# Performance work log

Hardware: AMD Instinct MI355X
Metric: run time of the kernel (lower is better)

The kernel has to match this reference:

```python
import jax, jax.numpy as jnp
import numpy as np

HIDDEN = 128
HEADS = 8
HEAD_DIM = HIDDEN // HEADS
N_BLOCKS = 2048
N_EDGES = 4096


def setup_inputs() -> dict:
    key = jax.random.key(0)
    ks = jax.random.split(key, 14)
    s = 0.02
    return {
        "block_features": jax.random.normal(ks[0], (N_BLOCKS, HIDDEN), dtype=jnp.float32),
        "edge_indices": jax.random.randint(ks[1], (2, N_EDGES), 0, N_BLOCKS, dtype=jnp.int32),
        # edge_encoder: Linear(2H->H), ReLU, Linear(H->H)
        "W_e1": jax.random.normal(ks[2], (2 * HIDDEN, HIDDEN), dtype=jnp.float32) * s,
        "b_e1": jnp.zeros((HIDDEN,), dtype=jnp.float32),
        "W_e2": jax.random.normal(ks[3], (HIDDEN, HIDDEN), dtype=jnp.float32) * s,
        "b_e2": jnp.zeros((HIDDEN,), dtype=jnp.float32),
        "Wq": jax.random.normal(ks[4], (HIDDEN, HIDDEN), dtype=jnp.float32) * s,
        "bq": jnp.zeros((HIDDEN,), dtype=jnp.float32),
        "Wk": jax.random.normal(ks[5], (HIDDEN, HIDDEN), dtype=jnp.float32) * s,
        "bk": jnp.zeros((HIDDEN,), dtype=jnp.float32),
        "Wv": jax.random.normal(ks[6], (HIDDEN, HIDDEN), dtype=jnp.float32) * s,
        "bv": jnp.zeros((HIDDEN,), dtype=jnp.float32),
        "Wo": jax.random.normal(ks[7], (HIDDEN, HIDDEN), dtype=jnp.float32) * s,
        "bo": jnp.zeros((HIDDEN,), dtype=jnp.float32),
    }


def reference(block_features, edge_indices, W_e1, b_e1, W_e2, b_e2,
              Wq, bq, Wk, bk, Wv, bv, Wo, bo):
    n_blocks = block_features.shape[0]
    src_idx, dst_idx = edge_indices[0], edge_indices[1]

    # gather src/dst node features, concat -> edge MLP (dropout is identity in eval)
    ef = jnp.concatenate([block_features[src_idx], block_features[dst_idx]], axis=1)  # [E, 2H]
    ef = jnp.maximum(ef @ W_e1 + b_e1, 0.0) @ W_e2 + b_e2  # [E, H]

    E = ef.shape[0]
    scale = HEAD_DIM ** -0.5
    q = (ef @ Wq + bq).reshape(E, HEADS, HEAD_DIM)
    k = (ef @ Wk + bk).reshape(E, HEADS, HEAD_DIM)
    v = (ef @ Wv + bv).reshape(E, HEADS, HEAD_DIM)

    # dense attention over all edges
    scores = jnp.einsum("ehd,fhd->hef", q, k) * scale  # [H, E, E]
    attn = jax.nn.softmax(scores, axis=-1)
    attn_out = jnp.einsum("hef,fhd->ehd", attn, v).reshape(E, HIDDEN)
    updated_edges = attn_out @ Wo + bo  # [E, H]

    # scatter_sum back to destination nodes
    block_updates = jax.ops.segment_sum(updated_edges, dst_idx, num_segments=n_blocks)
    return block_features + block_updates
```

## Files before the change

### kernel.cpp

```cpp
#include <hip/hip_runtime.h>
#include <hip/hip_bf16.h>

#define NB 2048
#define NE 4096
#define HID 128
#define NHEAD 8
#define HD 16

#define FPSCALE 1048576.0f
#define INV_FPSCALE (1.0f/1048576.0f)
#define QSCALE 0.36067376022224085f

typedef short s16x8 __attribute__((ext_vector_type(8)));
typedef float f32x4  __attribute__((ext_vector_type(4)));
typedef float f32x16 __attribute__((ext_vector_type(16)));

static __device__ __forceinline__ ushort f2bf(float x) {
    uint u = __builtin_bit_cast(uint, x);
    uint r = (u + 0x7fffu + ((u >> 16) & 1u)) >> 16;
    return (ushort)r;
}
static __device__ __forceinline__ uint pack2bf(float a, float b) {
    return (uint)f2bf(a) | ((uint)f2bf(b) << 16);
}
static __device__ __forceinline__ uint packrd(float a, float b) {
    uint ua = __builtin_bit_cast(uint, a) + 0x8000u;
    uint ub = __builtin_bit_cast(uint, b) + 0x8000u;
    return __builtin_amdgcn_perm(ub, ua, 0x07060302u);
}

__global__ __launch_bounds__(256) void convert_kernel(
    const float* __restrict__ We1, const float* __restrict__ We2,
    const float* __restrict__ Wq,  const float* __restrict__ Wk,
    const float* __restrict__ Wv,  const float* __restrict__ Wo,
    ushort* __restrict__ wb, int4* __restrict__ acc_zero)
{
    int i = blockIdx.x * 256 + threadIdx.x;
    if (i < 65536) acc_zero[i] = make_int4(0, 0, 0, 0);
    if (i < 32768) {
        int n = i >> 8, k = i & 255;
        wb[i] = f2bf(We1[k * HID + n]);
        return;
    }
    int j = i - 32768;
    int m = j >> 14;
    int r = j & 16383;
    int n = r >> 7, k = r & 127;
    const float* W = (m == 0) ? We2 : (m == 1) ? Wq : (m == 2) ? Wk : (m == 3) ? Wv : Wo;
    wb[i] = f2bf(W[k * HID + n]);
}

__global__ __launch_bounds__(512) void mlp_qkv_kernel(
    const float* __restrict__ bf, const int* __restrict__ src, const int* __restrict__ dst,
    const ushort* __restrict__ wb,
    const float* __restrict__ be1, const float* __restrict__ be2,
    const float* __restrict__ bq,  const float* __restrict__ bk, const float* __restrict__ bv,
    ushort* __restrict__ qg, ushort* __restrict__ kg, ushort* __restrict__ vT)
{
    __shared__ ushort sX[16][264];
    __shared__ ushort sH[16][136];
    __shared__ ushort sE[16][136];

    const int tid = threadIdx.x;
    const int w   = tid >> 6;
    const int l   = tid & 63;
    const int lo16 = l & 15;
    const int hi4  = l >> 4;
    const int e0 = blockIdx.x * 16;

    const ushort* We1T = wb;
    const ushort* We2T = wb + 32768;
    const ushort* WqT  = wb + 49152;
    const ushort* WkT  = wb + 65536;
    const ushort* WvT  = wb + 81920;

    {
        const int r  = tid >> 5;
        const int sg = tid & 31;
        const int e  = e0 + r;
        const int node = (sg < 16) ? src[e] : dst[e];
        const float4* rowp = (const float4*)(bf + node * HID);
        const int fb = (sg & 15) * 2;
        float4 t0 = rowp[fb], t1 = rowp[fb + 1];
        *(uint2*)&sX[r][sg * 8]     = make_uint2(pack2bf(t0.x, t0.y), pack2bf(t0.z, t0.w));
        *(uint2*)&sX[r][sg * 8 + 4] = make_uint2(pack2bf(t1.x, t1.y), pack2bf(t1.z, t1.w));
    }
    __syncthreads();

    f32x4 acc;

    {
        float b = be1[w * 16 + lo16];
        acc = (f32x4){b, b, b, b};
        #pragma unroll
        for (int k0 = 0; k0 < 8; k0++) {
            s16x8 a = *(const s16x8*)&sX[lo16][k0 * 32 + hi4 * 8];
            s16x8 bb = *(const s16x8*)(We1T + (w * 16 + lo16) * 256 + k0 * 32 + hi4 * 8);
            acc = __builtin_amdgcn_mfma_f32_16x16x32_bf16(a, bb, acc, 0, 0, 0);
        }
        #pragma unroll
        for (int r = 0; r < 4; r++)
            sH[hi4 * 4 + r][w * 16 + lo16] = f2bf(fmaxf(acc[r], 0.0f));
    }
    __syncthreads();

    {
        float b = be2[w * 16 + lo16];
        acc = (f32x4){b, b, b, b};
        #pragma unroll
        for (int k0 = 0; k0 < 4; k0++) {
            s16x8 a = *(const s16x8*)&sH[lo16][k0 * 32 + hi4 * 8];
            s16x8 bb = *(const s16x8*)(We2T + (w * 16 + lo16) * 128 + k0 * 32 + hi4 * 8);
            acc = __builtin_amdgcn_mfma_f32_16x16x32_bf16(a, bb, acc, 0, 0, 0);
        }
        #pragma unroll
        for (int r = 0; r < 4; r++)
            sE[hi4 * 4 + r][w * 16 + lo16] = f2bf(acc[r]);
    }
    __syncthreads();

#define PROJ(WT, BIAS, STORE) do { \
    float b_ = BIAS[w * 16 + lo16]; \
    acc = (f32x4){b_, b_, b_, b_}; \
    _Pragma("unroll") \
    for (int k0 = 0; k0 < 4; k0++) { \
        s16x8 a = *(const s16x8*)&sE[lo16][k0 * 32 + hi4 * 8]; \
        s16x8 bb = *(const s16x8*)(WT + (w * 16 + lo16) * 128 + k0 * 32 + hi4 * 8); \
        acc = __builtin_amdgcn_mfma_f32_16x16x32_bf16(a, bb, acc, 0, 0, 0); \
    } \
    _Pragma("unroll") \
    for (int r = 0; r < 4; r++) { STORE; } \
} while (0)

    PROJ(WqT, bq, { int e = e0 + hi4 * 4 + r;
                    qg[(w * NE + e) * 16 + lo16] = f2bf(acc[r] * QSCALE); });
    PROJ(WkT, bk, { int e = e0 + hi4 * 4 + r;
                    kg[(w * NE + e) * 16 + lo16] = f2bf(acc[r]); });
    PROJ(WvT, bv, { int e = e0 + hi4 * 4 + r;
                    vT[(w * 16 + lo16) * NE + e] = f2bf(acc[r]); });
#undef PROJ
}

__global__ __launch_bounds__(256) void attn_kernel(
    const ushort* __restrict__ qg, const ushort* __restrict__ kg,
    const ushort* __restrict__ vT, ushort* __restrict__ Og)
{
    __shared__ ushort P[4][2][8][32][4];
    __shared__ float sO[4][32][17];
    __shared__ float sL[4][2][32];

    const int tid = threadIdx.x;
    const int w   = tid >> 6;
    const int l   = tid & 63;
    const int h   = blockIdx.y;
    const int q0  = blockIdx.x * 32;
    const int lo16 = l & 15, hi4 = l >> 4;
    const int lo32 = l & 31, hi2 = l >> 5;

    const s16x8 qf = *(const s16x8*)(qg + (h * NE + q0 + lo32) * 16 + hi2 * 8);

    const f32x16 z16 = {0,0,0,0, 0,0,0,0, 0,0,0,0, 0,0,0,0};
    f32x4 o0 = {0,0,0,0}, o1 = {0,0,0,0};
    float L = 0.0f;

    const int kbase = w * (NE / 4);

    #pragma unroll 2
    for (int kt = 0; kt < NE / 4 / 32; kt++) {
        const int key0 = kbase + kt * 32;
        const int b = kt & 1;
        s16x8 kf = *(const s16x8*)(kg + (h * NE + key0 + lo32) * 16 + hi2 * 8);
        s16x8 vf = *(const s16x8*)(vT + (h * 16 + lo16) * NE + key0 + hi4 * 8);

        f32x16 s = __builtin_amdgcn_mfma_f32_32x32x16_bf16(kf, qf, z16, 0, 0, 0);

        float p[16];
        #pragma unroll
        for (int i = 0; i < 16; i++) { p[i] = __builtin_amdgcn_exp2f(s[i]); L += p[i]; }

        #pragma unroll
        for (int g = 0; g < 4; g++) {
            uint2 w2 = make_uint2(packrd(p[4*g], p[4*g+1]), packrd(p[4*g+2], p[4*g+3]));
            *(uint2*)&P[w][b][2*g + hi2][lo32][0] = w2;
        }

        uint2 alo = *(const uint2*)&P[w][b][2*hi4][lo16][0];
        uint2 ahi = *(const uint2*)&P[w][b][2*hi4 + 1][lo16][0];
        uint2 blo = *(const uint2*)&P[w][b][2*hi4][16 + lo16][0];
        uint2 bhi = *(const uint2*)&P[w][b][2*hi4 + 1][16 + lo16][0];
        uint4 ua = make_uint4(alo.x, alo.y, ahi.x, ahi.y);
        uint4 ub = make_uint4(blo.x, blo.y, bhi.x, bhi.y);
        s16x8 pb0 = __builtin_bit_cast(s16x8, ua);
        s16x8 pb1 = __builtin_bit_cast(s16x8, ub);
        o0 = __builtin_amdgcn_mfma_f32_16x16x32_bf16(vf, pb0, o0, 0, 0, 0);
        o1 = __builtin_amdgcn_mfma_f32_16x16x32_bf16(vf, pb1, o1, 0, 0, 0);
    }

    sL[w][hi2][lo32] = L;
    #pragma unroll
    for (int r = 0; r < 4; r++) {
        sO[w][lo16][hi4 * 4 + r]      = o0[r];
        sO[w][16 + lo16][hi4 * 4 + r] = o1[r];
    }
    __syncthreads();

    {
        const int q = tid >> 3;
        const int d0 = (tid & 7) * 2;
        float s0 = 0.0f, s1 = 0.0f, Lq = 0.0f;
        #pragma unroll
        for (int ww = 0; ww < 4; ww++) {
            s0 += sO[ww][q][d0];
            s1 += sO[ww][q][d0 + 1];
            Lq += sL[ww][0][q] + sL[ww][1][q];
        }
        float inv = 1.0f / Lq;
        *(uint*)&Og[(q0 + q) * HID + h * 16 + d0] = pack2bf(s0 * inv, s1 * inv);
    }
}

__global__ __launch_bounds__(512) void wo_scatter_kernel(
    const ushort* __restrict__ Og, const ushort* __restrict__ wb,
    const float* __restrict__ bo, const int* __restrict__ dst,
    int* __restrict__ acc_int)
{
    const int tid = threadIdx.x;
    const int w   = tid >> 6;
    const int l   = tid & 63;
    const int lo16 = l & 15, hi4 = l >> 4;
    const int e0 = blockIdx.x * 16;
    const ushort* WoT = wb + 98304;

    float b_ = bo[w * 16 + lo16];
    f32x4 acc = (f32x4){b_, b_, b_, b_};
    #pragma unroll
    for (int k0 = 0; k0 < 4; k0++) {
        s16x8 a = *(const s16x8*)(Og + (e0 + lo16) * HID + k0 * 32 + hi4 * 8);
        s16x8 bb = *(const s16x8*)(WoT + (w * 16 + lo16) * 128 + k0 * 32 + hi4 * 8);
        acc = __builtin_amdgcn_mfma_f32_16x16x32_bf16(a, bb, acc, 0, 0, 0);
    }

    #pragma unroll
    for (int r = 0; r < 4; r++) {
        int n = dst[e0 + hi4 * 4 + r];
        atomicAdd(acc_int + n * HID + w * 16 + lo16,
                  __float2int_rn(acc[r] * FPSCALE));
    }
}

__global__ __launch_bounds__(256) void finalize_kernel(
    const float4* __restrict__ bf, const int4* __restrict__ acc_int,
    float4* __restrict__ out)
{
    int i = blockIdx.x * 256 + threadIdx.x;
    float4 b = bf[i];
    int4   a = acc_int[i];
    out[i] = make_float4(b.x + (float)a.x * INV_FPSCALE,
                         b.y + (float)a.y * INV_FPSCALE,
                         b.z + (float)a.z * INV_FPSCALE,
                         b.w + (float)a.w * INV_FPSCALE);
}

extern "C" void kernel_launch(void* const* d_in, const int* in_sizes, int n_in,
                              void* d_out, int out_size, void* d_ws, size_t ws_size,
                              hipStream_t stream)
{
    const float* bf  = (const float*)d_in[0];
    const int*   ei  = (const int*)d_in[1];
    const int*   src = ei;
    const int*   dst = ei + NE;
    const float* We1 = (const float*)d_in[2];
    const float* be1 = (const float*)d_in[3];
    const float* We2 = (const float*)d_in[4];
    const float* be2 = (const float*)d_in[5];
    const float* Wq  = (const float*)d_in[6];
    const float* bq  = (const float*)d_in[7];
    const float* Wk  = (const float*)d_in[8];
    const float* bk  = (const float*)d_in[9];
    const float* Wv  = (const float*)d_in[10];
    const float* bv  = (const float*)d_in[11];
    const float* Wo  = (const float*)d_in[12];
    const float* bo  = (const float*)d_in[13];

    char* ws = (char*)d_ws;
    ushort* wb  = (ushort*)(ws);
    ushort* qg  = (ushort*)(ws + 229376);
    ushort* kg  = (ushort*)(ws + 229376 + (1u<<20));
    ushort* vT  = (ushort*)(ws + 229376 + (2u<<20));
    ushort* Og  = (ushort*)(ws + 229376 + (3u<<20));
    int*   acc  = (int*)  (ws + 229376 + (4u<<20));

    convert_kernel<<<448, 256, 0, stream>>>(We1, We2, Wq, Wk, Wv, Wo, wb, (int4*)acc);
    mlp_qkv_kernel<<<NE / 16, 512, 0, stream>>>(bf, src, dst, wb, be1, be2, bq, bk, bv,
                                                qg, kg, vT);
    attn_kernel<<<dim3(NE / 32, NHEAD), 256, 0, stream>>>(qg, kg, vT, Og);
    wo_scatter_kernel<<<NE / 16, 512, 0, stream>>>(Og, wb, bo, dst, acc);
    finalize_kernel<<<(NB * HID) / 1024, 256, 0, stream>>>((const float4*)bf, (const int4*)acc,
                                                           (float4*)d_out);
}
```

Measured before the change: 55.27 us.

## Compute softmax denominator via padded ones row in V MFMA, shuffle P in registers

V is stored transposed with 32 rows per head, where row 16 is filled with bf16 ones and the rest zero, so a single 32x32x16 MFMA yields both the P·V output and the row sum L. The P tile is rearranged into the MFMA B-operand layout through cross-half wave shuffles instead of an LDS round trip. The attention block grows to 8 waves, each covering 512 keys. This removes the scalar L accumulation and the per-iteration LDS traffic, at the cost of MFMA work on padding rows and twice the V storage.

```diff
diff --git a/kernel.cpp b/kernel.cpp
--- a/kernel.cpp
+++ b/kernel.cpp
@@ -33,10 +33,15 @@
     const float* __restrict__ We1, const float* __restrict__ We2,
     const float* __restrict__ Wq,  const float* __restrict__ Wk,
     const float* __restrict__ Wv,  const float* __restrict__ Wo,
-    ushort* __restrict__ wb, int4* __restrict__ acc_zero)
+    ushort* __restrict__ wb, int4* __restrict__ acc_zero, uint4* __restrict__ vfill)
 {
     int i = blockIdx.x * 256 + threadIdx.x;
-    if (i < 65536) acc_zero[i] = make_int4(0, 0, 0, 0);
+    if (i < 65536) {
+        acc_zero[i] = make_int4(0, 0, 0, 0);
+        int h = i >> 13, rr = (i >> 9) & 15, c = i & 511;
+        uint v = (rr == 0) ? 0x3f803f80u : 0u;
+        vfill[(h * 32 + 16 + rr) * 512 + c] = make_uint4(v, v, v, v);
+    }
     if (i < 32768) {
         int n = i >> 8, k = i & 255;
         wb[i] = f2bf(We1[k * HID + n]);
@@ -55,7 +60,7 @@
     const ushort* __restrict__ wb,
     const float* __restrict__ be1, const float* __restrict__ be2,
     const float* __restrict__ bq,  const float* __restrict__ bk, const float* __restrict__ bv,
-    ushort* __restrict__ qg, ushort* __restrict__ kg, ushort* __restrict__ vT)
+    ushort* __restrict__ qg, ushort* __restrict__ kg, ushort* __restrict__ vTx)
 {
     __shared__ ushort sX[16][264];
     __shared__ ushort sH[16][136];
@@ -137,85 +142,98 @@
     PROJ(WkT, bk, { int e = e0 + hi4 * 4 + r;
                     kg[(w * NE + e) * 16 + lo16] = f2bf(acc[r]); });
     PROJ(WvT, bv, { int e = e0 + hi4 * 4 + r;
-                    vT[(w * 16 + lo16) * NE + e] = f2bf(acc[r]); });
+                    vTx[(w * 32 + lo16) * NE + e] = f2bf(acc[r]); });
 #undef PROJ
 }
 
-__global__ __launch_bounds__(256) void attn_kernel(
+__global__ __launch_bounds__(512) void attn_kernel(
     const ushort* __restrict__ qg, const ushort* __restrict__ kg,
-    const ushort* __restrict__ vT, ushort* __restrict__ Og)
-{
-    __shared__ ushort P[4][2][8][32][4];
-    __shared__ float sO[4][32][17];
-    __shared__ float sL[4][2][32];
+    const ushort* __restrict__ vTx, ushort* __restrict__ Og)
+{
+    __shared__ float sO[8][32][18];
 
     const int tid = threadIdx.x;
     const int w   = tid >> 6;
     const int l   = tid & 63;
+    const int lo32 = l & 31, hi2 = l >> 5;
     const int h   = blockIdx.y;
     const int q0  = blockIdx.x * 32;
-    const int lo16 = l & 15, hi4 = l >> 4;
-    const int lo32 = l & 31, hi2 = l >> 5;
 
     const s16x8 qf = *(const s16x8*)(qg + (h * NE + q0 + lo32) * 16 + hi2 * 8);
-
-    const f32x16 z16 = {0,0,0,0, 0,0,0,0, 0,0,0,0, 0,0,0,0};
-    f32x4 o0 = {0,0,0,0}, o1 = {0,0,0,0};
-    float L = 0.0f;
-
-    const int kbase = w * (NE / 4);
+    const ushort* vbase = vTx + (size_t)(h * 32 + lo32) * NE + hi2 * 8;
+
+    const f32x16 z16 = {};
+    f32x16 accO = {};
 
     #pragma unroll 2
-    for (int kt = 0; kt < NE / 4 / 32; kt++) {
-        const int key0 = kbase + kt * 32;
-        const int b = kt & 1;
-        s16x8 kf = *(const s16x8*)(kg + (h * NE + key0 + lo32) * 16 + hi2 * 8);
-        s16x8 vf = *(const s16x8*)(vT + (h * 16 + lo16) * NE + key0 + hi4 * 8);
+    for (int kt = 0; kt < 16; kt++) {
+        const int key0 = w * 512 + kt * 32;
+        s16x8 kf  = *(const s16x8*)(kg + (h * NE + key0 + lo32) * 16 + hi2 * 8);
+        s16x8 va0 = *(const s16x8*)(vbase + key0);
+        s16x8 va1 = *(const s16x8*)(vbase + key0 + 16);
 
         f32x16 s = __builtin_amdgcn_mfma_f32_32x32x16_bf16(kf, qf, z16, 0, 0, 0);
 
-        float p[16];
-        #pragma unroll
-        for (int i = 0; i < 16; i++) { p[i] = __builtin_amdgcn_exp2f(s[i]); L += p[i]; }
-
-        #pragma unroll
-        for (int g = 0; g < 4; g++) {
-            uint2 w2 = make_uint2(packrd(p[4*g], p[4*g+1]), packrd(p[4*g+2], p[4*g+3]));
-            *(uint2*)&P[w][b][2*g + hi2][lo32][0] = w2;
-        }
-
-        uint2 alo = *(const uint2*)&P[w][b][2*hi4][lo16][0];
-        uint2 ahi = *(const uint2*)&P[w][b][2*hi4 + 1][lo16][0];
-        uint2 blo = *(const uint2*)&P[w][b][2*hi4][16 + lo16][0];
-        uint2 bhi = *(const uint2*)&P[w][b][2*hi4 + 1][16 + lo16][0];
-        uint4 ua = make_uint4(alo.x, alo.y, ahi.x, ahi.y);
-        uint4 ub = make_uint4(blo.x, blo.y, bhi.x, bhi.y);
-        s16x8 pb0 = __builtin_bit_cast(s16x8, ua);
-        s16x8 pb1 = __builtin_bit_cast(s16x8, ub);
-        o0 = __builtin_amdgcn_mfma_f32_16x16x32_bf16(vf, pb0, o0, 0, 0, 0);
-        o1 = __builtin_amdgcn_mfma_f32_16x16x32_bf16(vf, pb1, o1, 0, 0, 0);
-    }
-
-    sL[w][hi2][lo32] = L;
-    #pragma unroll
-    for (int r = 0; r < 4; r++) {
-        sO[w][lo16][hi4 * 4 + r]      = o0[r];
-        sO[w][16 + lo16][hi4 * 4 + r] = o1[r];
+        uint u0 = packrd(__builtin_amdgcn_exp2f(s[0]),  __builtin_amdgcn_exp2f(s[1]));
+        uint u1 = packrd(__builtin_amdgcn_exp2f(s[2]),  __builtin_amdgcn_exp2f(s[3]));
+        uint u2 = packrd(__builtin_amdgcn_exp2f(s[4]),  __builtin_amdgcn_exp2f(s[5]));
+        uint u3 = packrd(__builtin_amdgcn_exp2f(s[6]),  __builtin_amdgcn_exp2f(s[7]));
+        uint u4 = packrd(__builtin_amdgcn_exp2f(s[8]),  __builtin_amdgcn_exp2f(s[9]));
+        uint u5 = packrd(__builtin_amdgcn_exp2f(s[10]), __builtin_amdgcn_exp2f(s[11]));
+        uint u6 = packrd(__builtin_amdgcn_exp2f(s[12]), __builtin_amdgcn_exp2f(s[13]));
+        uint u7 = packrd(__builtin_amdgcn_exp2f(s[14]), __builtin_amdgcn_exp2f(s[15]));
+
+        uint up0 = (uint)__shfl_xor((int)u0, 32);
+        uint up1 = (uint)__shfl_xor((int)u1, 32);
+        uint up2 = (uint)__shfl_xor((int)u2, 32);
+        uint up3 = (uint)__shfl_xor((int)u3, 32);
+        uint up4 = (uint)__shfl_xor((int)u4, 32);
+        uint up5 = (uint)__shfl_xor((int)u5, 32);
+        uint up6 = (uint)__shfl_xor((int)u6, 32);
+        uint up7 = (uint)__shfl_xor((int)u7, 32);
+
+        uint b0, b1, b2, b3, b4, b5, b6, b7;
+        if (hi2 == 0) {
+            b0 = u0;  b1 = u1;  b2 = up0; b3 = up1;
+            b4 = u4;  b5 = u5;  b6 = up4; b7 = up5;
+        } else {
+            b0 = up2; b1 = up3; b2 = u2;  b3 = u3;
+            b4 = up6; b5 = up7; b6 = u6;  b7 = u7;
+        }
+        s16x8 f0 = __builtin_bit_cast(s16x8, make_uint4(b0, b1, b2, b3));
+        s16x8 f1 = __builtin_bit_cast(s16x8, make_uint4(b4, b5, b6, b7));
+
+        accO = __builtin_amdgcn_mfma_f32_32x32x16_bf16(va0, f0, accO, 0, 0, 0);
+        accO = __builtin_amdgcn_mfma_f32_32x32x16_bf16(va1, f1, accO, 0, 0, 0);
+    }
+
+    {
+        float* row = &sO[w][lo32][0];
+        if (hi2 == 0) {
+            *(float2*)&row[0]  = make_float2(accO[0], accO[1]);
+            *(float2*)&row[2]  = make_float2(accO[2], accO[3]);
+            *(float2*)&row[8]  = make_float2(accO[4], accO[5]);
+            *(float2*)&row[10] = make_float2(accO[6], accO[7]);
+            row[16] = accO[8];
+        } else {
+            *(float2*)&row[4]  = make_float2(accO[0], accO[1]);
+            *(float2*)&row[6]  = make_float2(accO[2], accO[3]);
+            *(float2*)&row[12] = make_float2(accO[4], accO[5]);
+            *(float2*)&row[14] = make_float2(accO[6], accO[7]);
+        }
     }
     __syncthreads();
 
     {
-        const int q = tid >> 3;
-        const int d0 = (tid & 7) * 2;
-        float s0 = 0.0f, s1 = 0.0f, Lq = 0.0f;
-        #pragma unroll
-        for (int ww = 0; ww < 4; ww++) {
-            s0 += sO[ww][q][d0];
-            s1 += sO[ww][q][d0 + 1];
-            Lq += sL[ww][0][q] + sL[ww][1][q];
-        }
-        float inv = 1.0f / Lq;
-        *(uint*)&Og[(q0 + q) * HID + h * 16 + d0] = pack2bf(s0 * inv, s1 * inv);
+        const int q = tid >> 4;
+        const int d = tid & 15;
+        float sum = 0.0f, Lq = 0.0f;
+        #pragma unroll
+        for (int ww = 0; ww < 8; ww++) {
+            sum += sO[ww][q][d];
+            Lq  += sO[ww][q][16];
+        }
+        Og[(q0 + q) * HID + h * 16 + d] = f2bf(sum / Lq);
     }
 }
 
@@ -284,16 +302,17 @@
 
     char* ws = (char*)d_ws;
     ushort* wb  = (ushort*)(ws);
-    ushort* qg  = (ushort*)(ws + 229376);
-    ushort* kg  = (ushort*)(ws + 229376 + (1u<<20));
-    ushort* vT  = (ushort*)(ws + 229376 + (2u<<20));
-    ushort* Og  = (ushort*)(ws + 229376 + (3u<<20));
-    int*   acc  = (int*)  (ws + 229376 + (4u<<20));
-
-    convert_kernel<<<448, 256, 0, stream>>>(We1, We2, Wq, Wk, Wv, Wo, wb, (int4*)acc);
+    ushort* qg  = (ushort*)(ws + (1u<<18));
+    ushort* kg  = (ushort*)(ws + (1u<<18) + (1u<<20));
+    ushort* vTx = (ushort*)(ws + (1u<<18) + (2u<<20));
+    ushort* Og  = (ushort*)(ws + (1u<<18) + (4u<<20));
+    int*   acc  = (int*)  (ws + (1u<<18) + (5u<<20));
+
+    convert_kernel<<<448, 256, 0, stream>>>(We1, We2, Wq, Wk, Wv, Wo, wb,
+                                            (int4*)acc, (uint4*)vTx);
     mlp_qkv_kernel<<<NE / 16, 512, 0, stream>>>(bf, src, dst, wb, be1, be2, bq, bk, bv,
-                                                qg, kg, vT);
-    attn_kernel<<<dim3(NE / 32, NHEAD), 256, 0, stream>>>(qg, kg, vT, Og);
+                                                qg, kg, vTx);
+    attn_kernel<<<dim3(NE / 32, NHEAD), 512, 0, stream>>>(qg, kg, vTx, Og);
     wo_scatter_kernel<<<NE / 16, 512, 0, stream>>>(Og, wb, bo, dst, acc);
     finalize_kernel<<<(NB * HID) / 1024, 256, 0, stream>>>((const float4*)bf, (const int4*)acc,
                                                            (float4*)d_out);
```

New measurement: 61.90 us. 1.12x slower.
